# Kernel tuning notes

Hardware: AMD Instinct MI355X
Metric: run time of the kernel (lower is better)

Reference implementation:

```python
import jax, jax.numpy as jnp
import numpy as np

NUM_HEAD = 16
D_MODEL = 1024
D_HEAD = D_MODEL // NUM_HEAD
BATCH = 4
SEQ = 2048


def setup_inputs() -> dict:
    key = jax.random.key(0)
    kq, kk, kv, kw, kb = jax.random.split(key, 5)
    Q = jax.random.normal(kq, (BATCH, SEQ, D_MODEL), dtype=jnp.float32)
    K = jax.random.normal(kk, (BATCH, SEQ, D_MODEL), dtype=jnp.float32)
    V = jax.random.normal(kv, (BATCH, SEQ, D_MODEL), dtype=jnp.float32)
    # nn.Linear weight [out, in] and bias [out]; scaled like torch default init
    Wq_w = jax.random.normal(kw, (D_MODEL, D_MODEL), dtype=jnp.float32) * (1.0 / np.sqrt(D_MODEL))
    Wq_b = jax.random.normal(kb, (D_MODEL,), dtype=jnp.float32) * 0.01
    return {"Q": Q, "K": K, "V": V, "Wq_w": Wq_w, "Wq_b": Wq_b}


def _split_head(x):
    # [b, s, d_model] -> [b, h, s, d_head]
    b, s, _ = x.shape
    return x.reshape(b, s, NUM_HEAD, D_HEAD).transpose(0, 2, 1, 3)


def reference(Q, K, V, Wq_w, Wq_b):
    # NOTE: original module (faithfully) uses Wq for all three projections.
    q = Q @ Wq_w.T + Wq_b
    k = K @ Wq_w.T + Wq_b
    v = V @ Wq_w.T + Wq_b
    q = _split_head(q)  # [b, h, s, dh]
    k = _split_head(k)
    v = _split_head(v)
    scale = 1.0 / jnp.sqrt(jnp.float32(D_HEAD))
    scores = jnp.einsum("bhqd,bhkd->bhqk", q, k) * scale  # [b, h, s, s]
    att_w = jax.nn.softmax(scores, axis=-1)
    out = jnp.einsum("bhqk,bhkd->bhqd", att_w, v)
    out = out.transpose(0, 2, 1, 3).reshape(Q.shape[0], -1, D_MODEL)
    return out, att_w
```

## Files before the change

kernel.cpp:

```cpp
#include <hip/hip_runtime.h>

typedef _Float16 f16;
typedef _Float16 f16x8 __attribute__((ext_vector_type(8)));
typedef _Float16 f16x4 __attribute__((ext_vector_type(4)));
typedef float    f32x4 __attribute__((ext_vector_type(4)));

static constexpr int NBATCH = 4;
static constexpr int NH     = 16;
static constexpr int SQ     = 2048;
static constexpr int DM     = 1024;
static constexpr int DHEAD  = 64;
static constexpr size_t TEL = (size_t)NBATCH * SQ * DM;
static constexpr size_t WEL = (size_t)DM * DM;

#define MFMA32(a, b, c) __builtin_amdgcn_mfma_f32_16x16x32_f16((a), (b), (c), 0, 0, 0)
#define MFMA16(a, b, c) __builtin_amdgcn_mfma_f32_16x16x16f16((a), (b), (c), 0, 0, 0)

#define GLOAD_LDS16(g, l)                                        \
    __builtin_amdgcn_global_load_lds(                            \
        (const __attribute__((address_space(1))) void*)(g),      \
        (__attribute__((address_space(3))) void*)(l), 16, 0, 0)

__global__ __launch_bounds__(256) void cvt_kernel(
    const float* __restrict__ X0, const float* __restrict__ X1,
    const float* __restrict__ X2, const float* __restrict__ W,
    f16* __restrict__ y0, f16* __restrict__ y1,
    f16* __restrict__ y2, f16* __restrict__ yw)
{
    constexpr int CX = (int)(TEL / 8);
    constexpr int CW = (int)(WEL / 8);
    const int total = 3 * CX + CW;
    for (int c = blockIdx.x * blockDim.x + threadIdx.x; c < total;
         c += gridDim.x * blockDim.x) {
        const float* src; f16* dst; int off;
        if (c < CX)            { src = X0; dst = y0; off = c; }
        else if (c < 2 * CX)   { src = X1; dst = y1; off = c - CX; }
        else if (c < 3 * CX)   { src = X2; dst = y2; off = c - 2 * CX; }
        else                   { src = W;  dst = yw; off = c - 3 * CX; }
        const float* p = src + (size_t)off * 8;
        float4 lo = *(const float4*)p;
        float4 hi = *(const float4*)(p + 4);
        f16x8 v;
        v[0] = (f16)lo.x; v[1] = (f16)lo.y; v[2] = (f16)lo.z; v[3] = (f16)lo.w;
        v[4] = (f16)hi.x; v[5] = (f16)hi.y; v[6] = (f16)hi.z; v[7] = (f16)hi.w;
        *(f16x8*)(dst + (size_t)off * 8) = v;
    }
}

__global__ __launch_bounds__(256, 2) void proj_kernel(
    const f16* __restrict__ X0, const f16* __restrict__ X1,
    const f16* __restrict__ X2, const f16* __restrict__ W,
    const float* __restrict__ bias,
    f16* __restrict__ wq, f16* __restrict__ wk, f16* __restrict__ wv)
{
    alignas(16) __shared__ f16 la[2][128 * 32];
    alignas(16) __shared__ f16 lb[2][128 * 32];

    const int bid   = blockIdx.x;
    const int which = bid / 512;
    const int t0    = bid % 512;
    const int nb    = t0 >> 6;
    const int mb    = t0 & 63;
    const f16* __restrict__ X  = (which == 0) ? X0 : (which == 1) ? X1 : X2;
    const f16* __restrict__ A0 = X + (size_t)mb * 128 * DM;
    const f16* __restrict__ B0 = W + (size_t)nb * 128 * DM;

    const int tid  = threadIdx.x;
    const int wave = tid >> 6;
    const int lane = tid & 63;
    const int wr   = wave >> 1, wc = wave & 1;
    const int l16  = lane & 15, g = lane >> 4;
    const int m_base = mb * 128 + wr * 64;
    const int n_base = nb * 128 + wc * 64;

    auto stage = [&](int buf, int k0) {
        #pragma unroll
        for (int half = 0; half < 2; ++half) {
            const int idx = half * 256 + wave * 64 + lane;
            const int row = idx >> 2;
            const int sc  = (idx & 3) ^ ((row >> 1) & 3);
            const int db  = (half * 256 + wave * 64) * 8;
            GLOAD_LDS16(A0 + (size_t)row * DM + k0 + sc * 8, &la[buf][db]);
            GLOAD_LDS16(B0 + (size_t)row * DM + k0 + sc * 8, &lb[buf][db]);
        }
    };

    f32x4 acc[4][4];
    #pragma unroll
    for (int i = 0; i < 4; ++i)
        #pragma unroll
        for (int j = 0; j < 4; ++j)
            acc[i][j] = (f32x4){0.f, 0.f, 0.f, 0.f};

    stage(0, 0);
    __syncthreads();
    for (int t = 0; t < 32; ++t) {
        const int buf = t & 1;
        if (t < 31) stage(buf ^ 1, (t + 1) * 32);
        f16x8 af[4], bf[4];
        #pragma unroll
        for (int qs = 0; qs < 4; ++qs) {
            const int row = wr * 64 + qs * 16 + l16;
            af[qs] = *(const f16x8*)&la[buf][row * 32 +
                                             ((g ^ ((row >> 1) & 3)) << 3)];
        }
        #pragma unroll
        for (int ns = 0; ns < 4; ++ns) {
            const int row = wc * 64 + ns * 16 + l16;
            bf[ns] = *(const f16x8*)&lb[buf][row * 32 +
                                             ((g ^ ((row >> 1) & 3)) << 3)];
        }
        #pragma unroll
        for (int qs = 0; qs < 4; ++qs)
            #pragma unroll
            for (int ns = 0; ns < 4; ++ns)
                acc[qs][ns] = MFMA32(af[qs], bf[ns], acc[qs][ns]);
        __syncthreads();
    }

    const int    s_base = m_base & (SQ - 1);
    const int    b      = m_base >> 11;
    const int    h      = nb * 2 + wc;
    const size_t bh     = (size_t)b * NH + h;

    float bv[4];
    #pragma unroll
    for (int ns = 0; ns < 4; ++ns) bv[ns] = bias[n_base + ns * 16 + l16];

    if (which == 2) {
        #pragma unroll
        for (int qs = 0; qs < 4; ++qs)
            #pragma unroll
            for (int ns = 0; ns < 4; ++ns) {
                f16x4 pk;
                #pragma unroll
                for (int r = 0; r < 4; ++r) pk[r] = (f16)(acc[qs][ns][r] + bv[ns]);
                const int dh = ns * 16 + l16;
                const int s0 = s_base + qs * 16 + 4 * g;
                *(f16x4*)(wv + (bh * DHEAD + dh) * SQ + s0) = pk;
            }
    } else {
        f16* __restrict__ dst = (which == 0) ? wq : wk;
        const float sc = (which == 0) ? 0.125f : 1.0f;
        #pragma unroll
        for (int qs = 0; qs < 4; ++qs)
            #pragma unroll
            for (int ns = 0; ns < 4; ++ns)
                #pragma unroll
                for (int r = 0; r < 4; ++r) {
                    const int s  = s_base + qs * 16 + 4 * g + r;
                    const int dh = ns * 16 + l16;
                    dst[(bh * SQ + s) * DHEAD + dh] =
                        (f16)((acc[qs][ns][r] + bv[ns]) * sc);
                }
    }
}

__global__ __launch_bounds__(256, 4) void attn_kernel(
    const f16* __restrict__ wq, const f16* __restrict__ wk,
    const f16* __restrict__ wv,
    float* __restrict__ out, float* __restrict__ att)
{
    alignas(16) __shared__ f16 lk[2][64 * 64];
    alignas(16) __shared__ f16 lv[2][64 * 64];

    const int tid  = threadIdx.x;
    const int wave = tid >> 6;
    const int lane = tid & 63;
    const int l16  = lane & 15, g = lane >> 4;

    const int bid     = blockIdx.x;
    const int logical = (bid & 7) * 128 + (bid >> 3);
    const int bh      = logical >> 4;
    const int q0      = (logical & 15) * 128 + wave * 32;

    const f16* __restrict__ qp = wq + (size_t)bh * SQ * DHEAD;
    const f16* __restrict__ kp = wk + (size_t)bh * SQ * DHEAD;
    const f16* __restrict__ vp = wv + (size_t)bh * DHEAD * SQ;
    float* __restrict__ attp = att + ((size_t)bh * SQ + q0) * SQ;
    const int b = bh >> 4, h = bh & 15;
    float* __restrict__ outp = out + ((size_t)b * SQ + q0) * DM + h * DHEAD;

    auto stage64 = [&](f16* dst0, const f16* gbase, int stride) {
        #pragma unroll
        for (int half = 0; half < 2; ++half) {
            const int idx = half * 256 + wave * 64 + lane;
            const int row = idx >> 3;
            const int sc  = (idx & 7) ^ (row & 7);
            GLOAD_LDS16(gbase + (size_t)row * stride + sc * 8,
                        dst0 + (size_t)(half * 256 + wave * 64) * 8);
        }
    };
    auto ldk8 = [&](int buf, int row, int c) -> f16x8 {
        return *(const f16x8*)&lk[buf][row * 64 + ((c ^ (row & 7)) << 3)];
    };
    auto ldv4 = [&](int buf, int row, int c_lin, int half8) -> f16x4 {
        return *(const f16x4*)&lv[buf][row * 64 + ((c_lin ^ (row & 7)) << 3) +
                                       half8 * 4];
    };

    f16x8 qf[2][2];
    #pragma unroll
    for (int qs = 0; qs < 2; ++qs)
        #pragma unroll
        for (int dhf = 0; dhf < 2; ++dhf)
            qf[qs][dhf] = *(const f16x8*)(qp + (size_t)(q0 + qs * 16 + l16) * DHEAD +
                                          dhf * 32 + g * 8);

    const f32x4 zero = (f32x4){0.f, 0.f, 0.f, 0.f};
    constexpr int NT = SQ / 64;

    float accl[2] = {0.f, 0.f};
    f32x4 oacc[2][4];
    #pragma unroll
    for (int qs = 0; qs < 2; ++qs)
        #pragma unroll
        for (int ds = 0; ds < 4; ++ds) oacc[qs][ds] = zero;

    stage64(&lk[0][0], kp, DHEAD);
    stage64(&lv[0][0], vp, SQ);
    __syncthreads();
    for (int t = 0; t < NT; ++t) {
        const int buf = t & 1;
        if (t + 1 < NT) {
            stage64(&lk[buf ^ 1][0], kp + (size_t)(t + 1) * 64 * DHEAD, DHEAD);
            stage64(&lv[buf ^ 1][0], vp + (t + 1) * 64, SQ);
        }
        #pragma unroll
        for (int s16 = 0; s16 < 4; ++s16) {
            const int row = s16 * 16 + l16;
            f16x8 kf0 = ldk8(buf, row, g);
            f16x8 kf1 = ldk8(buf, row, 4 + g);
            f16x4 pb[2];
            #pragma unroll
            for (int qs = 0; qs < 2; ++qs) {
                f32x4 sc = MFMA32(kf0, qf[qs][0], zero);
                sc = MFMA32(kf1, qf[qs][1], sc);
                float e0 = __expf(sc[0]), e1 = __expf(sc[1]);
                float e2 = __expf(sc[2]), e3 = __expf(sc[3]);
                accl[qs] += (e0 + e1) + (e2 + e3);
                f16x4 p; p[0] = (f16)e0; p[1] = (f16)e1;
                p[2] = (f16)e2; p[3] = (f16)e3;
                pb[qs] = p;
            }
            #pragma unroll
            for (int ds = 0; ds < 4; ++ds) {
                f16x4 vf = ldv4(buf, ds * 16 + l16, s16 * 2 + (g >> 1), g & 1);
                oacc[0][ds] = MFMA16(vf, pb[0], oacc[0][ds]);
                oacc[1][ds] = MFMA16(vf, pb[1], oacc[1][ds]);
            }
        }
        __syncthreads();
    }

    float linv[2];
    #pragma unroll
    for (int qs = 0; qs < 2; ++qs) {
        float v = accl[qs];
        v += __shfl_xor(v, 16, 64);
        v += __shfl_xor(v, 32, 64);
        linv[qs] = 1.f / v;
    }

    #pragma unroll
    for (int qs = 0; qs < 2; ++qs)
        #pragma unroll
        for (int ds = 0; ds < 4; ++ds) {
            float4 o;
            o.x = oacc[qs][ds][0] * linv[qs];
            o.y = oacc[qs][ds][1] * linv[qs];
            o.z = oacc[qs][ds][2] * linv[qs];
            o.w = oacc[qs][ds][3] * linv[qs];
            *(float4*)(outp + (size_t)(qs * 16 + l16) * DM + ds * 16 + 4 * g) = o;
        }

    stage64(&lk[0][0], kp, DHEAD);
    __syncthreads();
    for (int t = 0; t < NT; ++t) {
        const int buf = t & 1;
        const int kv0 = t * 64;
        if (t + 1 < NT)
            stage64(&lk[buf ^ 1][0], kp + (size_t)(t + 1) * 64 * DHEAD, DHEAD);
        #pragma unroll
        for (int s16 = 0; s16 < 4; ++s16) {
            const int row = s16 * 16 + l16;
            f16x8 kf0 = ldk8(buf, row, g);
            f16x8 kf1 = ldk8(buf, row, 4 + g);
            #pragma unroll
            for (int qs = 0; qs < 2; ++qs) {
                f32x4 sc = MFMA32(kf0, qf[qs][0], zero);
                sc = MFMA32(kf1, qf[qs][1], sc);
                float4 a;
                a.x = __expf(sc[0]) * linv[qs];
                a.y = __expf(sc[1]) * linv[qs];
                a.z = __expf(sc[2]) * linv[qs];
                a.w = __expf(sc[3]) * linv[qs];
                *(float4*)(attp + (size_t)(qs * 16 + l16) * SQ + kv0 +
                           s16 * 16 + 4 * g) = a;
            }
        }
        __syncthreads();
    }
}

extern "C" void kernel_launch(void* const* d_in, const int* in_sizes, int n_in,
                              void* d_out, int out_size, void* d_ws, size_t ws_size,
                              hipStream_t stream) {
    const float* Q    = (const float*)d_in[0];
    const float* K    = (const float*)d_in[1];
    const float* V    = (const float*)d_in[2];
    const float* W    = (const float*)d_in[3];
    const float* bias = (const float*)d_in[4];

    f16* wq = (f16*)d_ws;
    f16* wk = wq + TEL;
    f16* wv = wk + TEL;

    float* out = (float*)d_out;
    float* att = out + TEL;

    f16* x0 = (f16*)att;
    f16* x1 = x0 + TEL;
    f16* x2 = x1 + TEL;
    f16* xw = x2 + TEL;

    cvt_kernel <<<2048, 256, 0, stream>>>(Q, K, V, W, x0, x1, x2, xw);
    proj_kernel<<<1536, 256, 0, stream>>>(x0, x1, x2, xw, bias, wq, wk, wv);
    attn_kernel<<<1024, 256, 0, stream>>>(wq, wk, wv, out, att);
}
```

Measured before the change: 442.4 us.

## Fold log2e into Q scale, use exp2, and load K directly in att-write pass

The softmax scale now includes log2(e) in the Q projection epilogue, so the attention kernel can use the hardware exp2 instruction instead of __expf. The second pass that writes the attention-weight matrix no longer stages K through LDS with barriers. Each lane instead loads its K fragments straight from global memory, prefetching one 16-row step ahead. The projection kernel's launch bounds are raised to three blocks per CU to improve occupancy, at the risk of register spills.

After: 595.1 us. 1.35x slower.

```diff
diff --git a/kernel.cpp b/kernel.cpp
--- a/kernel.cpp
+++ b/kernel.cpp
@@ -13,8 +13,11 @@
 static constexpr size_t TEL = (size_t)NBATCH * SQ * DM;
 static constexpr size_t WEL = (size_t)DM * DM;
 
+static constexpr float QSCALE = 0.125f * 1.4426950408889634f;
+
 #define MFMA32(a, b, c) __builtin_amdgcn_mfma_f32_16x16x32_f16((a), (b), (c), 0, 0, 0)
 #define MFMA16(a, b, c) __builtin_amdgcn_mfma_f32_16x16x16f16((a), (b), (c), 0, 0, 0)
+#define EXP2(x) __builtin_amdgcn_exp2f(x)
 
 #define GLOAD_LDS16(g, l)                                        \
     __builtin_amdgcn_global_load_lds(                            \
@@ -47,7 +50,7 @@
     }
 }
 
-__global__ __launch_bounds__(256, 2) void proj_kernel(
+__global__ __launch_bounds__(256, 3) void proj_kernel(
     const f16* __restrict__ X0, const f16* __restrict__ X1,
     const f16* __restrict__ X2, const f16* __restrict__ W,
     const float* __restrict__ bias,
@@ -141,7 +144,7 @@
             }
     } else {
         f16* __restrict__ dst = (which == 0) ? wq : wk;
-        const float sc = (which == 0) ? 0.125f : 1.0f;
+        const float sc = (which == 0) ? QSCALE : 1.0f;
         #pragma unroll
         for (int qs = 0; qs < 4; ++qs)
             #pragma unroll
@@ -236,8 +239,8 @@
             for (int qs = 0; qs < 2; ++qs) {
                 f32x4 sc = MFMA32(kf0, qf[qs][0], zero);
                 sc = MFMA32(kf1, qf[qs][1], sc);
-                float e0 = __expf(sc[0]), e1 = __expf(sc[1]);
-                float e2 = __expf(sc[2]), e3 = __expf(sc[3]);
+                float e0 = EXP2(sc[0]), e1 = EXP2(sc[1]);
+                float e2 = EXP2(sc[2]), e3 = EXP2(sc[3]);
                 accl[qs] += (e0 + e1) + (e2 + e3);
                 f16x4 p; p[0] = (f16)e0; p[1] = (f16)e1;
                 p[2] = (f16)e2; p[3] = (f16)e3;
@@ -274,32 +277,30 @@
             *(float4*)(outp + (size_t)(qs * 16 + l16) * DM + ds * 16 + 4 * g) = o;
         }
 
-    stage64(&lk[0][0], kp, DHEAD);
-    __syncthreads();
-    for (int t = 0; t < NT; ++t) {
-        const int buf = t & 1;
-        const int kv0 = t * 64;
-        if (t + 1 < NT)
-            stage64(&lk[buf ^ 1][0], kp + (size_t)(t + 1) * 64 * DHEAD, DHEAD);
-        #pragma unroll
-        for (int s16 = 0; s16 < 4; ++s16) {
-            const int row = s16 * 16 + l16;
-            f16x8 kf0 = ldk8(buf, row, g);
-            f16x8 kf1 = ldk8(buf, row, 4 + g);
+    {
+        const f16* prow = kp + (size_t)l16 * DHEAD + g * 8;
+        f16x8 nkf0 = *(const f16x8*)prow;
+        f16x8 nkf1 = *(const f16x8*)(prow + 32);
+        for (int kv16 = 0; kv16 < SQ / 16; ++kv16) {
+            f16x8 kf0 = nkf0, kf1 = nkf1;
+            if (kv16 + 1 < SQ / 16) {
+                const f16* p = kp + (size_t)((kv16 + 1) * 16 + l16) * DHEAD + g * 8;
+                nkf0 = *(const f16x8*)p;
+                nkf1 = *(const f16x8*)(p + 32);
+            }
             #pragma unroll
             for (int qs = 0; qs < 2; ++qs) {
                 f32x4 sc = MFMA32(kf0, qf[qs][0], zero);
                 sc = MFMA32(kf1, qf[qs][1], sc);
                 float4 a;
-                a.x = __expf(sc[0]) * linv[qs];
-                a.y = __expf(sc[1]) * linv[qs];
-                a.z = __expf(sc[2]) * linv[qs];
-                a.w = __expf(sc[3]) * linv[qs];
-                *(float4*)(attp + (size_t)(qs * 16 + l16) * SQ + kv0 +
-                           s16 * 16 + 4 * g) = a;
-            }
-        }
-        __syncthreads();
+                a.x = EXP2(sc[0]) * linv[qs];
+                a.y = EXP2(sc[1]) * linv[qs];
+                a.z = EXP2(sc[2]) * linv[qs];
+                a.w = EXP2(sc[3]) * linv[qs];
+                *(float4*)(attp + (size_t)(qs * 16 + l16) * SQ +
+                           kv16 * 16 + 4 * g) = a;
+            }
+        }
     }
 }
 
```
